# Kernel optimization log

Measured on AMD Instinct MI355X. Metric: run time of the kernel, lower is better.

Reference implementation:

```python
import jax, jax.numpy as jnp
import numpy as np

B, S, D, H = 4, 2048, 1024, 16
DK = D // H


def setup_inputs() -> dict:
    key = jax.random.key(0)
    ks = jax.random.split(key, 10)
    std = 0.02
    inp = {
        "input": jax.random.normal(ks[0], (B, S, D), dtype=jnp.float32),
        "attention_reweight": jax.random.uniform(ks[1], (B, S), dtype=jnp.float32),
        "mask": 1,
        "Wq": jax.random.normal(ks[2], (D, D), dtype=jnp.float32) * std,
        "bq": jnp.zeros((D,), dtype=jnp.float32),
        "Wk": jax.random.normal(ks[3], (D, D), dtype=jnp.float32) * std,
        "bk": jnp.zeros((D,), dtype=jnp.float32),
        "Wv": jax.random.normal(ks[4], (D, D), dtype=jnp.float32) * std,
        "bv": jnp.zeros((D,), dtype=jnp.float32),
        "Wo": jax.random.normal(ks[5], (D, D), dtype=jnp.float32) * std,
        "bo": jnp.zeros((D,), dtype=jnp.float32),
    }
    return inp


def reference(input, attention_reweight, mask, Wq, bq, Wk, bk, Wv, bv, Wo, bo):
    b, s, d = input.shape
    # QKV projections (torch Linear: x @ W.T + b)
    q = (input @ Wq.T + bq).reshape(b, s, H, DK).transpose(0, 2, 1, 3)  # [B,H,S,dk]
    k = (input @ Wk.T + bk).reshape(b, s, H, DK).transpose(0, 2, 1, 3)
    v = (input @ Wv.T + bv).reshape(b, s, H, DK).transpose(0, 2, 1, 3)

    scores = jnp.einsum("bhqd,bhkd->bhqk", q, k)  # [B,H,S,S]
    if mask:
        causal = jnp.triu(jnp.ones((s, s), dtype=scores.dtype), k=1)
        scores = scores - causal * 1e9
    scores = scores / jnp.sqrt(jnp.asarray(DK, dtype=jnp.float32))
    # reweight per key position: [B,S] broadcast over heads and query positions
    scores = scores * attention_reweight[:, None, None, :]

    attn = jax.nn.softmax(scores, axis=-1)
    out = jnp.einsum("bhqk,bhkd->bhqd", attn, v)  # [B,H,S,dk]
    out = out.transpose(0, 2, 1, 3).reshape(b, s, d)
    return out @ Wo.T + bo
```

## Files before the change

### kernel.cpp

```cpp
#include <hip/hip_runtime.h>
#include <math.h>

#define B_  4
#define S_  2048
#define D_  1024
#define H_  16
#define DK_ 64

typedef __bf16 bf16x8 __attribute__((ext_vector_type(8)));
typedef float  f32x4  __attribute__((ext_vector_type(4)));

__device__ __forceinline__ unsigned short f2bf(float f) {
  unsigned int u = __builtin_bit_cast(unsigned int, f);
  u += 0x7fffu + ((u >> 16) & 1u);
  return (unsigned short)(u >> 16);
}

__device__ __forceinline__ unsigned short bfbits(float f) {
  __bf16 h = (__bf16)f;
  return __builtin_bit_cast(unsigned short, h);
}

__device__ __forceinline__ f32x4 mfma16(bf16x8 a, bf16x8 b, f32x4 c) {
  return __builtin_amdgcn_mfma_f32_16x16x32_bf16(a, b, c, 0, 0, 0);
}

__device__ __forceinline__ void gl_lds16(const unsigned short* g, unsigned short* l) {
  __builtin_amdgcn_global_load_lds(
      (const __attribute__((address_space(1))) void*)g,
      (__attribute__((address_space(3))) void*)l, 16, 0, 0);
}

__device__ __forceinline__ bf16x8 pack8(float4 a, float4 b) {
  bf16x8 r;
  r[0] = (__bf16)a.x; r[1] = (__bf16)a.y; r[2] = (__bf16)a.z; r[3] = (__bf16)a.w;
  r[4] = (__bf16)b.x; r[5] = (__bf16)b.y; r[6] = (__bf16)b.z; r[7] = (__bf16)b.w;
  return r;
}

__global__ void SAA_cast4(const float* __restrict__ s0, const float* __restrict__ s1,
                          const float* __restrict__ s2, const float* __restrict__ s3,
                          unsigned short* __restrict__ d0, unsigned short* __restrict__ d1,
                          unsigned short* __restrict__ d2, unsigned short* __restrict__ d3)
{
  const int y = blockIdx.y;
  const float* src = (y == 0) ? s0 : (y == 1) ? s1 : (y == 2) ? s2 : s3;
  unsigned short* dst = (y == 0) ? d0 : (y == 1) ? d1 : (y == 2) ? d2 : d3;
  const int n4 = (D_ * D_) / 4;
  int i = blockIdx.x * blockDim.x + threadIdx.x;
  int stride = gridDim.x * blockDim.x;
  for (; i < n4; i += stride) {
    float4 v = reinterpret_cast<const float4*>(src)[i];
    ushort4 o;
    o.x = f2bf(v.x); o.y = f2bf(v.y); o.z = f2bf(v.z); o.w = f2bf(v.w);
    reinterpret_cast<ushort4*>(dst)[i] = o;
  }
}

__global__ __launch_bounds__(512)
void SAA_gemm_qkv(const float* __restrict__ Xf,
                  const unsigned short* __restrict__ Wqb,
                  const unsigned short* __restrict__ Wkb,
                  const unsigned short* __restrict__ Wvb,
                  const float* __restrict__ bq,
                  const float* __restrict__ bk,
                  const float* __restrict__ bv,
                  const float* __restrict__ rw,
                  unsigned short* __restrict__ Qo,
                  unsigned short* __restrict__ Ko,
                  unsigned short* __restrict__ Vto)
{
  const int K = D_;
  __shared__ __attribute__((aligned(16))) unsigned short smem[65536];
#define sAp(sl)     (smem + (sl) * 8192)
#define sBp(sl, m)  (smem + 16384 + ((sl) * 3 + (m)) * 8192)

  const int t = threadIdx.x;
  const int w = t >> 6, l = t & 63;
  const int wm = w >> 2, wn = w & 3;
  const int lr = l & 15, lg = l >> 4;
  const int r7 = lr & 7;

  const int bid = blockIdx.x;
  const int m0 = (bid >> 3) * 128;
  const int n0 = (bid & 7) * 128;

  const float* gA = Xf + (size_t)m0 * K;
  const unsigned short* gB0 = Wqb + (size_t)n0 * K;
  const unsigned short* gB1 = Wkb + (size_t)n0 * K;
  const unsigned short* gB2 = Wvb + (size_t)n0 * K;

  int srow[2], soff[2];
#pragma unroll
  for (int i = 0; i < 2; i++) {
    const int c = i * 512 + t;
    srow[i] = c >> 3;
    soff[i] = ((c & 7) ^ (srow[i] & 7)) * 8;
  }

  float4 a4[2][2];

#define LOADA(k0)                                                             \
  do {                                                                        \
    _Pragma("unroll")                                                         \
    for (int i = 0; i < 2; i++) {                                             \
      const float* p = gA + (size_t)srow[i] * K + (k0) + soff[i];             \
      a4[i][0] = *reinterpret_cast<const float4*>(p);                         \
      a4[i][1] = *reinterpret_cast<const float4*>(p + 4);                     \
    }                                                                         \
  } while (0)

#define WRITEA(s)                                                             \
  do {                                                                        \
    _Pragma("unroll")                                                         \
    for (int i = 0; i < 2; i++)                                               \
      *reinterpret_cast<bf16x8*>(sAp(s) + (i * 512 + t) * 8) =                \
          pack8(a4[i][0], a4[i][1]);                                          \
  } while (0)

#define STAGEB(s, k0)                                                         \
  do {                                                                        \
    _Pragma("unroll")                                                         \
    for (int i = 0; i < 2; i++) {                                             \
      const size_t go = (size_t)srow[i] * K + (k0) + soff[i];                 \
      const int dl = (i * 512 + t) * 8;                                       \
      gl_lds16(gB0 + go, sBp(s, 0) + dl);                                     \
      gl_lds16(gB1 + go, sBp(s, 1) + dl);                                     \
      gl_lds16(gB2 + go, sBp(s, 2) + dl);                                     \
    }                                                                         \
  } while (0)

  LOADA(0);
  STAGEB(0, 0);
  WRITEA(0);

  f32x4 acc[3][4][2] = {};

#pragma unroll 2
  for (int T = 0; T < 16; ++T) {
    __syncthreads();
    if (T + 1 < 16) { LOADA((T + 1) * 64); STAGEB((T + 1) & 1, (T + 1) * 64); }

    const unsigned short* At = sAp(T & 1);
#pragma unroll
    for (int ks = 0; ks < 2; ++ks) {
      const int swk = (((ks * 4 + lg) ^ r7) << 3);
      bf16x8 afr[4];
#pragma unroll
      for (int mi = 0; mi < 4; ++mi)
        afr[mi] = *reinterpret_cast<const bf16x8*>(
            &At[(wm * 64 + mi * 16 + lr) * 64 + swk]);
#pragma unroll
      for (int mat = 0; mat < 3; ++mat) {
        const unsigned short* Bt = sBp(T & 1, mat);
        bf16x8 bfr[2];
#pragma unroll
        for (int n = 0; n < 2; ++n)
          bfr[n] = *reinterpret_cast<const bf16x8*>(
              &Bt[(wn * 32 + n * 16 + lr) * 64 + swk]);
#pragma unroll
        for (int mi = 0; mi < 4; ++mi)
#pragma unroll
          for (int n = 0; n < 2; ++n)
            acc[mat][mi][n] = mfma16(afr[mi], bfr[n], acc[mat][mi][n]);
      }
    }

    if (T + 1 < 16) WRITEA((T + 1) & 1);
  }
#undef LOADA
#undef WRITEA
#undef STAGEB

  __syncthreads();

#pragma unroll
  for (int n = 0; n < 2; ++n) {
    const int col = n0 + wn * 32 + n * 16 + lr;
    const int h = col >> 6, dk = col & 63;
    const float bvv = bv[col];
#pragma unroll
    for (int mi = 0; mi < 4; ++mi) {
      const int row0 = m0 + wm * 64 + mi * 16 + lg * 4;
      const int b = row0 >> 11, s0 = row0 & 2047;
      ushort4 pk;
      pk.x = bfbits(acc[2][mi][n][0] + bvv);
      pk.y = bfbits(acc[2][mi][n][1] + bvv);
      pk.z = bfbits(acc[2][mi][n][2] + bvv);
      pk.w = bfbits(acc[2][mi][n][3] + bvv);
      *reinterpret_cast<ushort4*>(
          &Vto[(((size_t)b * H_ + h) * DK_ + dk) * S_ + s0]) = pk;
    }
  }

  unsigned short* bounce = smem;
  for (int mat = 0; mat < 2; ++mat) {
    const float* bias = mat ? bk : bq;
#pragma unroll
    for (int n = 0; n < 2; ++n) {
      const int col = n0 + wn * 32 + n * 16 + lr;
      const int lcol = wn * 32 + n * 16 + lr;
      const float bs = bias[col];
#pragma unroll
      for (int mi = 0; mi < 4; ++mi) {
#pragma unroll
        for (int r = 0; r < 4; ++r) {
          const int lrow = wm * 64 + mi * 16 + lg * 4 + r;
          float v = acc[mat][mi][n][r] + bs;
          if (mat) v *= 0.18033688011112042f * rw[m0 + lrow];
          bounce[lrow * 132 + lcol] = bfbits(v);
        }
      }
    }
    __syncthreads();
#pragma unroll
    for (int i = 0; i < 2; ++i) {
      const int idx = i * 512 + t;
      const int lrow = idx >> 3, c16 = (idx & 7) * 16;
      const int row = m0 + lrow;
      const int b = row >> 11, s = row & 2047;
      const int col = n0 + c16;
      const int h = col >> 6, dk = col & 63;
      const unsigned short* srcp = &bounce[lrow * 132 + c16];
      unsigned short* dst = (mat ? Ko : Qo) + (((size_t)b * H_ + h) * S_ + s) * DK_ + dk;
#pragma unroll
      for (int j = 0; j < 4; ++j)
        reinterpret_cast<ushort4*>(dst)[j] =
            reinterpret_cast<const ushort4*>(srcp)[j];
    }
    __syncthreads();
  }
#undef sAp
#undef sBp
}

__global__ __launch_bounds__(512)
void SAA_attn(const unsigned short* __restrict__ Q,
              const unsigned short* __restrict__ Kb,
              const unsigned short* __restrict__ Vt,
              const int* __restrict__ maskp,
              unsigned short* __restrict__ Cb)
{
  const int L = (blockIdx.x & 7) * 64 + (blockIdx.x >> 3);
  const int pairid = L & 7;
  const int h = (L >> 3) & 15;
  const int b = L >> 7;

  const int t = threadIdx.x, w = t >> 6, l = t & 63;
  const int lr = l & 15, lg = l >> 4;
  const int mask = maskp[0];

  __shared__ __attribute__((aligned(16))) unsigned short Kt[2][64 * 64];
  __shared__ __attribute__((aligned(16))) unsigned short Vl[2][64 * 64];
  __shared__ __attribute__((aligned(16))) unsigned short Pl[8][16 * 80];

  const size_t bh = (size_t)b * H_ + h;
  const unsigned short* Qbh = Q + bh * S_ * DK_;
  const unsigned short* Kbh = Kb + bh * S_ * DK_;
  const unsigned short* Vbh = Vt + bh * DK_ * S_;
  unsigned short* Pw = &Pl[w][0];

  const int r0 = t >> 3, cc0 = t & 7;
  const int sw0 = (cc0 ^ (r0 & 7)) * 8;

  for (int half = 0; half < 2; ++half) {
    const int qb = half ? (15 - pairid) : pairid;
    const int q0 = qb * 128;
    const int wq = q0 + w * 16;

    bf16x8 qf[2];
#pragma unroll
    for (int ks = 0; ks < 2; ks++)
      qf[ks] = *reinterpret_cast<const bf16x8*>(
          &Qbh[(size_t)(wq + lr) * DK_ + ks * 32 + lg * 8]);

    f32x4 acc[4] = {};
    float lrun[4] = {0.f, 0.f, 0.f, 0.f};

    const int nkt = mask ? (qb * 2 + 2) : (S_ / 64);
    const int wqmax = wq + 15;

    __syncthreads();

    gl_lds16(Kbh + (size_t)r0 * DK_ + sw0, &Kt[0][t * 8]);
    gl_lds16(Vbh + (size_t)r0 * S_ + sw0,  &Vl[0][t * 8]);
    int cur = 0;

    for (int kt = 0; kt < nkt; ++kt) {
      __syncthreads();
      if (kt + 1 < nkt) {
        const int kn = (kt + 1) * 64;
        const int nb = cur ^ 1;
        gl_lds16(Kbh + (size_t)(kn + r0) * DK_ + sw0, &Kt[nb][t * 8]);
        gl_lds16(Vbh + (size_t)r0 * S_ + kn + sw0,    &Vl[nb][t * 8]);
      }

      const int k0 = kt * 64;
      const bool active = (!mask) || (k0 <= wqmax);
      if (active) {
        const unsigned short* Kc = &Kt[cur][0];
        const unsigned short* Vc = &Vl[cur][0];

        __builtin_amdgcn_s_setprio(1);
        f32x4 sc[4] = {};
#pragma unroll
        for (int ks = 0; ks < 2; ++ks) {
          const int swk = (((ks * 4 + lg) ^ (lr & 7)) << 3);
#pragma unroll
          for (int t2 = 0; t2 < 4; ++t2) {
            bf16x8 kf = *reinterpret_cast<const bf16x8*>(&Kc[(t2 * 16 + lr) * 64 + swk]);
            sc[t2] = mfma16(qf[ks], kf, sc[t2]);
          }
        }
        __builtin_amdgcn_s_setprio(0);

        const bool needmask = mask && (k0 + 63 > wq);

#pragma unroll
        for (int r = 0; r < 4; r++) {
          const int row = wq + lg * 4 + r;
          float v0 = sc[0][r], v1 = sc[1][r];
          float v2 = sc[2][r], v3 = sc[3][r];
          if (needmask) {
            if (k0 + lr      > row) v0 = -1e30f;
            if (k0 + 16 + lr > row) v1 = -1e30f;
            if (k0 + 32 + lr > row) v2 = -1e30f;
            if (k0 + 48 + lr > row) v3 = -1e30f;
          }
          const float p0 = __builtin_amdgcn_exp2f(v0);
          const float p1 = __builtin_amdgcn_exp2f(v1);
          const float p2 = __builtin_amdgcn_exp2f(v2);
          const float p3 = __builtin_amdgcn_exp2f(v3);
          lrun[r] += (p0 + p1) + (p2 + p3);
          unsigned short* pp = &Pw[(lg * 4 + r) * 80 + lr];
          pp[0]  = bfbits(p0);
          pp[16] = bfbits(p1);
          pp[32] = bfbits(p2);
          pp[48] = bfbits(p3);
        }

        __builtin_amdgcn_s_setprio(1);
#pragma unroll
        for (int ks = 0; ks < 2; ++ks) {
          const int swk = (((ks * 4 + lg) ^ (lr & 7)) << 3);
          bf16x8 pf = *reinterpret_cast<const bf16x8*>(&Pw[lr * 80 + ks * 32 + lg * 8]);
#pragma unroll
          for (int dt = 0; dt < 4; ++dt) {
            bf16x8 vf = *reinterpret_cast<const bf16x8*>(&Vc[(dt * 16 + lr) * 64 + swk]);
            acc[dt] = mfma16(pf, vf, acc[dt]);
          }
        }
        __builtin_amdgcn_s_setprio(0);
      }
      cur ^= 1;
    }

#pragma unroll
    for (int r = 0; r < 4; r++) {
      float rs = lrun[r];
      rs += __shfl_xor(rs, 1);
      rs += __shfl_xor(rs, 2);
      rs += __shfl_xor(rs, 4);
      rs += __shfl_xor(rs, 8);
      lrun[r] = __builtin_amdgcn_rcpf(rs);
    }
#pragma unroll
    for (int dt = 0; dt < 4; dt++) {
#pragma unroll
      for (int r = 0; r < 4; r++) {
        const int row = wq + lg * 4 + r;
        const int col = h * DK_ + dt * 16 + lr;
        Cb[((size_t)b * S_ + row) * D_ + col] = bfbits(acc[dt][r] * lrun[r]);
      }
    }
  }
}

__global__ __launch_bounds__(512)
void SAA_gemm_out(const unsigned short* __restrict__ Cb,
                  const unsigned short* __restrict__ Wob,
                  const float* __restrict__ bo,
                  float* __restrict__ Y)
{
  const int K = D_;
  __shared__ __attribute__((aligned(16))) unsigned short lA[2][512 * 64];
  __shared__ __attribute__((aligned(16))) unsigned short lB[2][64 * 64];

  const int L = (blockIdx.x & 7) * 32 + (blockIdx.x >> 3);
  const int nx = L & 15, my = L >> 4;

  const int t = threadIdx.x;
  const int w = t >> 6, l = t & 63;
  const int lr = l & 15, lg = l >> 4;
  const int r7 = lr & 7;

  const int m0 = my * 512;
  const int n0 = nx * 64;

  const unsigned short* gA = Cb + (size_t)m0 * K;
  const unsigned short* gB = Wob + (size_t)n0 * K;

  const int sr = t >> 3;
  const int soff = ((t & 7) ^ (sr & 7)) * 8;

#define STAGEO(s, k0)                                                         \
  do {                                                                        \
    _Pragma("unroll")                                                         \
    for (int i = 0; i < 8; i++)                                               \
      gl_lds16(gA + (size_t)(i * 64 + sr) * K + (k0) + soff,                  \
               &lA[s][(i * 512 + t) * 8]);                                    \
    gl_lds16(gB + (size_t)sr * K + (k0) + soff, &lB[s][t * 8]);               \
  } while (0)

  STAGEO(0, 0);

  f32x4 acc[4][4] = {};

#pragma unroll 2
  for (int T = 0; T < 16; ++T) {
    __syncthreads();
    if (T + 1 < 16) STAGEO((T + 1) & 1, (T + 1) * 64);

    const unsigned short* At = lA[T & 1];
    const unsigned short* Bt = lB[T & 1];
#pragma unroll
    for (int ks = 0; ks < 2; ks++) {
      const int swk = (((ks * 4 + lg) ^ r7) << 3);
      bf16x8 af[4], bfr[4];
#pragma unroll
      for (int i = 0; i < 4; i++)
        af[i] = *reinterpret_cast<const bf16x8*>(&At[(w * 64 + i * 16 + lr) * 64 + swk]);
#pragma unroll
      for (int j = 0; j < 4; j++)
        bfr[j] = *reinterpret_cast<const bf16x8*>(&Bt[(j * 16 + lr) * 64 + swk]);
#pragma unroll
      for (int i = 0; i < 4; i++)
#pragma unroll
        for (int j = 0; j < 4; j++)
          acc[i][j] = mfma16(af[i], bfr[j], acc[i][j]);
    }
  }
#undef STAGEO

#pragma unroll
  for (int j = 0; j < 4; j++) {
    const int col = n0 + j * 16 + lr;
    const float bsv = bo[col];
#pragma unroll
    for (int i = 0; i < 4; i++) {
#pragma unroll
      for (int r = 0; r < 4; r++) {
        const int row = m0 + w * 64 + i * 16 + lg * 4 + r;
        Y[(size_t)row * D_ + col] = acc[i][j][r] + bsv;
      }
    }
  }
}

extern "C" void kernel_launch(void* const* d_in, const int* in_sizes, int n_in,
                              void* d_out, int out_size, void* d_ws, size_t ws_size,
                              hipStream_t stream) {
  const float* input = (const float*)d_in[0];
  const float* rw    = (const float*)d_in[1];
  const int*   maskp = (const int*)d_in[2];
  const float* Wq = (const float*)d_in[3];
  const float* bq = (const float*)d_in[4];
  const float* Wk = (const float*)d_in[5];
  const float* bk = (const float*)d_in[6];
  const float* Wv = (const float*)d_in[7];
  const float* bv = (const float*)d_in[8];
  const float* Wo = (const float*)d_in[9];
  const float* bo = (const float*)d_in[10];

  char* ws = (char*)d_ws;
  unsigned short* Xb  = (unsigned short*)(ws);
  unsigned short* Wqb = (unsigned short*)(ws + (16u << 20));
  unsigned short* Wkb = (unsigned short*)(ws + (18u << 20));
  unsigned short* Wvb = (unsigned short*)(ws + (20u << 20));
  unsigned short* Wob = (unsigned short*)(ws + (22u << 20));
  unsigned short* Qo  = (unsigned short*)(ws + (24u << 20));
  unsigned short* Ko  = (unsigned short*)(ws + (40u << 20));
  unsigned short* Vto = (unsigned short*)(ws + (56u << 20));
  unsigned short* Cb  = Xb;

  SAA_cast4<<<dim3(512, 4), 256, 0, stream>>>(Wq, Wk, Wv, Wo, Wqb, Wkb, Wvb, Wob);

  SAA_gemm_qkv<<<512, 512, 0, stream>>>(input, Wqb, Wkb, Wvb, bq, bk, bv, rw,
                                        Qo, Ko, Vto);
  SAA_attn<<<512, 512, 0, stream>>>(Qo, Ko, Vto, maskp, Cb);
  SAA_gemm_out<<<256, 512, 0, stream>>>(Cb, Wob, bo, (float*)d_out);
}
```

Measured before the change: 168.1 us.

## Pre-cast input to bf16 and enlarge QKV GEMM M-tile with direct LDS loads

Adds a separate kernel that converts the fp32 input to bf16 ahead of time, so the QKV GEMM can stream A through global_load_lds instead of loading and packing fp32 in registers. The GEMM M-tile doubles to 256 rows, and the K step halves to 32 with a new swizzle. This increases reuse of the weight tiles and halves the grid. The extra cast pass adds memory traffic, and the larger accumulator set raises register pressure and lowers parallelism.

```diff
diff --git a/kernel.cpp b/kernel.cpp
--- a/kernel.cpp
+++ b/kernel.cpp
@@ -31,11 +31,16 @@
       (__attribute__((address_space(3))) void*)l, 16, 0, 0);
 }
 
-__device__ __forceinline__ bf16x8 pack8(float4 a, float4 b) {
-  bf16x8 r;
-  r[0] = (__bf16)a.x; r[1] = (__bf16)a.y; r[2] = (__bf16)a.z; r[3] = (__bf16)a.w;
-  r[4] = (__bf16)b.x; r[5] = (__bf16)b.y; r[6] = (__bf16)b.z; r[7] = (__bf16)b.w;
-  return r;
+__global__ void SAA_cast_bf16(const float* __restrict__ src,
+                              unsigned short* __restrict__ dst, int n4) {
+  int i = blockIdx.x * blockDim.x + threadIdx.x;
+  int stride = gridDim.x * blockDim.x;
+  for (; i < n4; i += stride) {
+    float4 v = reinterpret_cast<const float4*>(src)[i];
+    ushort4 o;
+    o.x = f2bf(v.x); o.y = f2bf(v.y); o.z = f2bf(v.z); o.w = f2bf(v.w);
+    reinterpret_cast<ushort4*>(dst)[i] = o;
+  }
 }
 
 __global__ void SAA_cast4(const float* __restrict__ s0, const float* __restrict__ s1,
@@ -58,7 +63,7 @@
 }
 
 __global__ __launch_bounds__(512)
-void SAA_gemm_qkv(const float* __restrict__ Xf,
+void SAA_gemm_qkv(const unsigned short* __restrict__ Xb,
                   const unsigned short* __restrict__ Wqb,
                   const unsigned short* __restrict__ Wkb,
                   const unsigned short* __restrict__ Wvb,
@@ -71,106 +76,81 @@
                   unsigned short* __restrict__ Vto)
 {
   const int K = D_;
-  __shared__ __attribute__((aligned(16))) unsigned short smem[65536];
+  __shared__ __attribute__((aligned(16))) unsigned short smem[40960];
 #define sAp(sl)     (smem + (sl) * 8192)
-#define sBp(sl, m)  (smem + 16384 + ((sl) * 3 + (m)) * 8192)
+#define sBp(sl, m)  (smem + 16384 + ((sl) * 3 + (m)) * 4096)
 
   const int t = threadIdx.x;
   const int w = t >> 6, l = t & 63;
   const int wm = w >> 2, wn = w & 3;
   const int lr = l & 15, lg = l >> 4;
-  const int r7 = lr & 7;
 
   const int bid = blockIdx.x;
-  const int m0 = (bid >> 3) * 128;
+  const int m0 = (bid >> 3) * 256;
   const int n0 = (bid & 7) * 128;
 
-  const float* gA = Xf + (size_t)m0 * K;
+  const unsigned short* gA  = Xb  + (size_t)m0 * K;
   const unsigned short* gB0 = Wqb + (size_t)n0 * K;
   const unsigned short* gB1 = Wkb + (size_t)n0 * K;
   const unsigned short* gB2 = Wvb + (size_t)n0 * K;
 
-  int srow[2], soff[2];
+  int sarow[2], saoff[2];
 #pragma unroll
   for (int i = 0; i < 2; i++) {
     const int c = i * 512 + t;
-    srow[i] = c >> 3;
-    soff[i] = ((c & 7) ^ (srow[i] & 7)) * 8;
-  }
-
-  float4 a4[2][2];
-
-#define LOADA(k0)                                                             \
-  do {                                                                        \
-    _Pragma("unroll")                                                         \
-    for (int i = 0; i < 2; i++) {                                             \
-      const float* p = gA + (size_t)srow[i] * K + (k0) + soff[i];             \
-      a4[i][0] = *reinterpret_cast<const float4*>(p);                         \
-      a4[i][1] = *reinterpret_cast<const float4*>(p + 4);                     \
-    }                                                                         \
-  } while (0)
-
-#define WRITEA(s)                                                             \
+    sarow[i] = c >> 2;
+    saoff[i] = ((c & 3) ^ ((sarow[i] >> 1) & 3)) * 8;
+  }
+  const int sbrow = t >> 2;
+  const int sboff = ((t & 3) ^ ((sbrow >> 1) & 3)) * 8;
+
+#define STAGE(s, k0)                                                          \
   do {                                                                        \
     _Pragma("unroll")                                                         \
     for (int i = 0; i < 2; i++)                                               \
-      *reinterpret_cast<bf16x8*>(sAp(s) + (i * 512 + t) * 8) =                \
-          pack8(a4[i][0], a4[i][1]);                                          \
+      gl_lds16(gA + (size_t)sarow[i] * K + (k0) + saoff[i],                   \
+               sAp(s) + (i * 512 + t) * 8);                                   \
+    const size_t gob = (size_t)sbrow * K + (k0) + sboff;                      \
+    gl_lds16(gB0 + gob, sBp(s, 0) + t * 8);                                   \
+    gl_lds16(gB1 + gob, sBp(s, 1) + t * 8);                                   \
+    gl_lds16(gB2 + gob, sBp(s, 2) + t * 8);                                   \
   } while (0)
 
-#define STAGEB(s, k0)                                                         \
-  do {                                                                        \
-    _Pragma("unroll")                                                         \
-    for (int i = 0; i < 2; i++) {                                             \
-      const size_t go = (size_t)srow[i] * K + (k0) + soff[i];                 \
-      const int dl = (i * 512 + t) * 8;                                       \
-      gl_lds16(gB0 + go, sBp(s, 0) + dl);                                     \
-      gl_lds16(gB1 + go, sBp(s, 1) + dl);                                     \
-      gl_lds16(gB2 + go, sBp(s, 2) + dl);                                     \
-    }                                                                         \
-  } while (0)
-
-  LOADA(0);
-  STAGEB(0, 0);
-  WRITEA(0);
-
-  f32x4 acc[3][4][2] = {};
+  STAGE(0, 0);
+
+  f32x4 acc[3][8][2] = {};
 
 #pragma unroll 2
-  for (int T = 0; T < 16; ++T) {
+  for (int T = 0; T < 32; ++T) {
     __syncthreads();
-    if (T + 1 < 16) { LOADA((T + 1) * 64); STAGEB((T + 1) & 1, (T + 1) * 64); }
+    if (T + 1 < 32) STAGE((T + 1) & 1, (T + 1) * 32);
 
     const unsigned short* At = sAp(T & 1);
-#pragma unroll
-    for (int ks = 0; ks < 2; ++ks) {
-      const int swk = (((ks * 4 + lg) ^ r7) << 3);
-      bf16x8 afr[4];
-#pragma unroll
-      for (int mi = 0; mi < 4; ++mi)
-        afr[mi] = *reinterpret_cast<const bf16x8*>(
-            &At[(wm * 64 + mi * 16 + lr) * 64 + swk]);
-#pragma unroll
-      for (int mat = 0; mat < 3; ++mat) {
-        const unsigned short* Bt = sBp(T & 1, mat);
-        bf16x8 bfr[2];
+    bf16x8 afr[8];
+#pragma unroll
+    for (int mi = 0; mi < 8; ++mi) {
+      const int row = wm * 128 + mi * 16 + lr;
+      afr[mi] = *reinterpret_cast<const bf16x8*>(
+          &At[row * 32 + ((lg ^ ((row >> 1) & 3)) << 3)]);
+    }
+#pragma unroll
+    for (int mat = 0; mat < 3; ++mat) {
+      const unsigned short* Bt = sBp(T & 1, mat);
+      bf16x8 bfr[2];
+#pragma unroll
+      for (int n = 0; n < 2; ++n) {
+        const int row = wn * 32 + n * 16 + lr;
+        bfr[n] = *reinterpret_cast<const bf16x8*>(
+            &Bt[row * 32 + ((lg ^ ((row >> 1) & 3)) << 3)]);
+      }
+#pragma unroll
+      for (int mi = 0; mi < 8; ++mi)
 #pragma unroll
         for (int n = 0; n < 2; ++n)
-          bfr[n] = *reinterpret_cast<const bf16x8*>(
-              &Bt[(wn * 32 + n * 16 + lr) * 64 + swk]);
-#pragma unroll
-        for (int mi = 0; mi < 4; ++mi)
-#pragma unroll
-          for (int n = 0; n < 2; ++n)
-            acc[mat][mi][n] = mfma16(afr[mi], bfr[n], acc[mat][mi][n]);
-      }
-    }
-
-    if (T + 1 < 16) WRITEA((T + 1) & 1);
-  }
-#undef LOADA
-#undef WRITEA
-#undef STAGEB
+          acc[mat][mi][n] = mfma16(afr[mi], bfr[n], acc[mat][mi][n]);
+    }
+  }
+#undef STAGE
 
   __syncthreads();
 
@@ -180,8 +160,8 @@
     const int h = col >> 6, dk = col & 63;
     const float bvv = bv[col];
 #pragma unroll
-    for (int mi = 0; mi < 4; ++mi) {
-      const int row0 = m0 + wm * 64 + mi * 16 + lg * 4;
+    for (int mi = 0; mi < 8; ++mi) {
+      const int row0 = m0 + wm * 128 + mi * 16 + lg * 4;
       const int b = row0 >> 11, s0 = row0 & 2047;
       ushort4 pk;
       pk.x = bfbits(acc[2][mi][n][0] + bvv);
@@ -202,10 +182,10 @@
       const int lcol = wn * 32 + n * 16 + lr;
       const float bs = bias[col];
 #pragma unroll
-      for (int mi = 0; mi < 4; ++mi) {
+      for (int mi = 0; mi < 8; ++mi) {
 #pragma unroll
         for (int r = 0; r < 4; ++r) {
-          const int lrow = wm * 64 + mi * 16 + lg * 4 + r;
+          const int lrow = wm * 128 + mi * 16 + lg * 4 + r;
           float v = acc[mat][mi][n][r] + bs;
           if (mat) v *= 0.18033688011112042f * rw[m0 + lrow];
           bounce[lrow * 132 + lcol] = bfbits(v);
@@ -214,7 +194,7 @@
     }
     __syncthreads();
 #pragma unroll
-    for (int i = 0; i < 2; ++i) {
+    for (int i = 0; i < 4; ++i) {
       const int idx = i * 512 + t;
       const int lrow = idx >> 3, c16 = (idx & 7) * 16;
       const int row = m0 + lrow;
@@ -483,9 +463,10 @@
   unsigned short* Vto = (unsigned short*)(ws + (56u << 20));
   unsigned short* Cb  = Xb;
 
+  SAA_cast_bf16<<<2048, 256, 0, stream>>>(input, Xb, (B_ * S_ * D_) / 4);
   SAA_cast4<<<dim3(512, 4), 256, 0, stream>>>(Wq, Wk, Wv, Wo, Wqb, Wkb, Wvb, Wob);
 
-  SAA_gemm_qkv<<<512, 512, 0, stream>>>(input, Wqb, Wkb, Wvb, bq, bk, bv, rw,
+  SAA_gemm_qkv<<<256, 512, 0, stream>>>(Xb, Wqb, Wkb, Wvb, bq, bk, bv, rw,
                                         Qo, Ko, Vto);
   SAA_attn<<<512, 512, 0, stream>>>(Qo, Ko, Vto, maskp, Cb);
   SAA_gemm_out<<<256, 512, 0, stream>>>(Cb, Wob, bo, (float*)d_out);
```

Result: faster. 162.2 us (-3.5%).
